# Kernel optimization log

Measured on AMD Instinct MI355X. Metric: run time of the kernel, lower is better.

The kernel has to match this reference:

```python
import jax, jax.numpy as jnp
import numpy as np

NUM_ITERATIONS = 3
EPS = 1e-12


def _squash(s):
    # s: (..., V). squash(s) = |s|^2 * s / ((1+|s|^2) * |s|)
    sq = jnp.sum(s * s, axis=-1, keepdims=True)
    return sq * s / ((1.0 + sq) * jnp.sqrt(sq))


def setup_inputs() -> dict:
    key = jax.random.key(0)
    kx, kw = jax.random.split(key)
    B, L, P, V, Q = 16, 64, 1024, 64, 16
    x = jax.random.normal(kx, (B, P, Q), dtype=jnp.float32)
    W = 0.01 * jax.random.normal(kw, (L, P, V, Q), dtype=jnp.float32)
    return {"x": x, "W": W}


def reference(x, W):
    # u_hat[b,l,p,v] = sum_q W[l,p,v,q] * x[b,p,q]
    u_hat = jnp.einsum('lpvq,bpq->blpv', W, x)  # (B, L, P, V)
    B, L, P, V = u_hat.shape
    b_ij = jnp.zeros((B, L, P), dtype=u_hat.dtype)
    c_ij = None
    v = None
    for it in range(NUM_ITERATIONS):  # small fixed unroll
        c_ij = jax.nn.softmax(b_ij, axis=1)  # softmax over latent caps
        s = jnp.einsum('blp,blpv->blv', c_ij, u_hat)
        v = _squash(s)  # (B, L, V)
        if it < NUM_ITERATIONS - 1:
            # agreement update: b_ij += <v_j, u_hat>
            b_ij = b_ij + jnp.einsum('blv,blpv->blp', v, u_hat)
    # T-score: coupling entropy over latent axis, per primary capsule
    cT = jnp.swapaxes(c_ij, 1, 2)  # (B, P, L)
    entropy = -jnp.sum(cT * jnp.log(cT + EPS), axis=-1)  # (B, P)
    T = jnp.mean(1.0 - entropy / np.log(float(L)))
    # D-score: max over caps of population std (over batch) of activation norms
    v_norm = jnp.linalg.norm(v, axis=-1)  # (B, L)
    D = jnp.max(jnp.std(v_norm, axis=0))
    return v, T, D
```

## Files before the change

kernel.cpp:

```cpp
#include <hip/hip_runtime.h>
#include <hip/hip_bf16.h>

#define B 16
#define L 64
#define P 1024
#define V 64
#define Q 16
#define LN64 4.158883083359672f

#define CHBC 16
#define NCH_BC (P / CHBC)

typedef unsigned short ushort8_t __attribute__((ext_vector_type(8)));

typedef const __attribute__((address_space(1))) void* gld_gptr_t;
typedef __attribute__((address_space(3))) void* gld_lptr_t;

static __device__ __forceinline__ float bf2f(ushort u) {
    return __uint_as_float(((unsigned int)u) << 16);
}
static __device__ __forceinline__ ushort f2bf(float f) {
    unsigned int x = __float_as_uint(f);
    unsigned int r = (x + 0x7fffu + ((x >> 16) & 1u)) >> 16;
    return (ushort)r;
}
static __device__ __forceinline__ float pklo(unsigned int w) {
    return __uint_as_float(w << 16);
}
static __device__ __forceinline__ float pkhi(unsigned int w) {
    return __uint_as_float(w & 0xffff0000u);
}

static __device__ __forceinline__ float wsum64(float v) {
#pragma unroll
    for (int m = 32; m > 0; m >>= 1) v += __shfl_xor(v, m, 64);
    return v;
}
static __device__ __forceinline__ float wmax64(float v) {
#pragma unroll
    for (int m = 32; m > 0; m >>= 1) v = fmaxf(v, __shfl_xor(v, m, 64));
    return v;
}

__global__ __launch_bounds__(256) void k_uhat(const float* __restrict__ Wt,
                                              const float* __restrict__ x,
                                              ushort* __restrict__ uhat) {
    const int t = threadIdx.x;
    const int w = t >> 6;
    const int lane = t & 63;
    const int p = blockIdx.x >> 1;
    const int l0 = (blockIdx.x & 1) * 32;

    __shared__ float xs[B * Q];
    __shared__ float wls[4][1024];

    {
        const int b = t >> 4, q = t & 15;
        xs[t] = x[((size_t)b * P + p) * Q + q];
    }
    __syncthreads();

    unsigned int xp[4][8];
#pragma unroll
    for (int i = 0; i < 4; ++i) {
        const int b = w * 4 + i;
#pragma unroll
        for (int j = 0; j < 8; ++j) {
            unsigned int lo = f2bf(xs[b * Q + 2 * j]);
            unsigned int hi = f2bf(xs[b * Q + 2 * j + 1]);
            xp[i][j] = lo | (hi << 16);
        }
    }

    const int i_idx = w * 64 + lane;
    const int src_chunk = (i_idx & ~3) | ((i_idx & 3) ^ ((i_idx >> 3) & 3));
    const char* gW = (const char*)Wt + ((size_t)l0 * P + p) * (V * Q * 4)
                     + (size_t)src_chunk * 16;
    const size_t LSTRIDE = (size_t)P * V * Q * 4;
    const int xsw = (lane >> 1) & 3;

#define STAGE(li)                                                             \
    __builtin_amdgcn_global_load_lds(                                         \
        (gld_gptr_t)(gW + (size_t)(li) * LSTRIDE),                            \
        (gld_lptr_t)&wls[(li) & 3][w * 256], 16, 0, 0);

#define COMPUTE(li)                                                           \
    {                                                                         \
        const char* sb = (const char*)&wls[(li) & 3][0] + lane * 64;          \
        float4 Wr[4];                                                         \
        Wr[0] = *(const float4*)(sb + ((0 ^ xsw) << 4));                      \
        Wr[1] = *(const float4*)(sb + ((1 ^ xsw) << 4));                      \
        Wr[2] = *(const float4*)(sb + ((2 ^ xsw) << 4));                      \
        Wr[3] = *(const float4*)(sb + ((3 ^ xsw) << 4));                      \
        _Pragma("unroll")                                                     \
        for (int i = 0; i < 4; ++i) {                                         \
            float u = 0.f;                                                    \
            _Pragma("unroll")                                                 \
            for (int j = 0; j < 8; ++j) {                                     \
                const float4 Wq = Wr[j >> 1];                                 \
                const float wlo = (j & 1) ? Wq.z : Wq.x;                      \
                const float whi = (j & 1) ? Wq.w : Wq.y;                      \
                u = fmaf(wlo, pklo(xp[i][j]), u);                             \
                u = fmaf(whi, pkhi(xp[i][j]), u);                             \
            }                                                                 \
            uhat[(((size_t)((w * 4 + i) * L + l0 + (li))) * P + p) * V + lane] \
                = f2bf(u);                                                    \
        }                                                                     \
    }

#define SYNC(N)                                                               \
    asm volatile("s_waitcnt vmcnt(" #N ")" ::: "memory");                     \
    __builtin_amdgcn_sched_barrier(0);                                        \
    __builtin_amdgcn_s_barrier();                                             \
    __builtin_amdgcn_sched_barrier(0);

    STAGE(0);
    STAGE(1);

    SYNC(1);
    STAGE(2);
    COMPUTE(0);
    SYNC(5);
    STAGE(3);
    COMPUTE(1);

#pragma unroll 1
    for (int li = 2; li <= 29; ++li) {
        SYNC(9);
        STAGE(li + 2);
        COMPUTE(li);
    }

    SYNC(9);
    COMPUTE(30);
    SYNC(8);
    COMPUTE(31);

#undef STAGE
#undef COMPUTE
#undef SYNC
}

__global__ __launch_bounds__(256) void k_s(const ushort* __restrict__ uhat,
                                           float* __restrict__ vout) {
    const int l = blockIdx.x, b = blockIdx.y;
    const int t = threadIdx.x;
    const int w = t >> 6, lane = t & 63;
    const int pl = t >> 4;
    const int vg = t & 15;

    __shared__ float4 sl[4][16];

    const ushort* up = uhat + ((size_t)(b * L + l)) * P * V + (size_t)pl * V + vg * 4;

    float4 acc = {0.f, 0.f, 0.f, 0.f};
#pragma unroll 8
    for (int i = 0; i < 64; ++i) {
        ushort4 u = *reinterpret_cast<const ushort4*>(up + (size_t)i * 16 * V);
        acc.x += bf2f(u.x); acc.y += bf2f(u.y);
        acc.z += bf2f(u.z); acc.w += bf2f(u.w);
    }
    acc.x *= (1.f / 64.f); acc.y *= (1.f / 64.f);
    acc.z *= (1.f / 64.f); acc.w *= (1.f / 64.f);
#pragma unroll
    for (int m = 16; m <= 32; m <<= 1) {
        acc.x += __shfl_xor(acc.x, m, 64);
        acc.y += __shfl_xor(acc.y, m, 64);
        acc.z += __shfl_xor(acc.z, m, 64);
        acc.w += __shfl_xor(acc.w, m, 64);
    }
    if (lane < 16) sl[w][vg] = acc;
    __syncthreads();
    if (w == 0 && lane < 16) {
        float4 s0 = sl[0][vg], s1 = sl[1][vg], s2 = sl[2][vg], s3 = sl[3][vg];
        float4 s;
        s.x = s0.x + s1.x + s2.x + s3.x;
        s.y = s0.y + s1.y + s2.y + s3.y;
        s.z = s0.z + s1.z + s2.z + s3.z;
        s.w = s0.w + s1.w + s2.w + s3.w;
        float sq = s.x * s.x + s.y * s.y + s.z * s.z + s.w * s.w;
        sq += __shfl_xor(sq, 1, 64);
        sq += __shfl_xor(sq, 2, 64);
        sq += __shfl_xor(sq, 4, 64);
        sq += __shfl_xor(sq, 8, 64);
        float f = sqrtf(sq) / (1.0f + sq);
        float4 o = {s.x * f, s.y * f, s.z * f, s.w * f};
        *reinterpret_cast<float4*>(vout + (size_t)(b * L + l) * V + vg * 4) = o;
    }
}

__global__ __launch_bounds__(512, 4) void k_bc(const ushort* __restrict__ uhat,
                                               const float* __restrict__ vv,
                                               float* __restrict__ bbuf,
                                               float* __restrict__ sp,
                                               float* __restrict__ Tsum,
                                               int add_prev, int do_T) {
    const int ch = blockIdx.x, b = blockIdx.y;
    const int p0 = ch * CHBC;
    const int t = threadIdx.x;
    const int w = t >> 6, lane = t & 63;
    const int pl8 = lane >> 3;
    const int vg8 = lane & 7;
    const int l0 = w * 8;

    __shared__ float vsh[L][V];
    __shared__ float bl[CHBC][L + 1];
    __shared__ float twv[8];

    {
        const float4* vvp = reinterpret_cast<const float4*>(vv + (size_t)b * L * V);
        float4* vshp = reinterpret_cast<float4*>(&vsh[0][0]);
#pragma unroll
        for (int i = 0; i < 2; ++i) vshp[t + i * 512] = vvp[t + i * 512];
    }

    ushort8_t ur[8][2];
    {
        const ushort* ubase = uhat + (((size_t)(b * L + l0)) * P + p0 + pl8) * V + vg8 * 8;
#pragma unroll
        for (int li = 0; li < 8; ++li) {
#pragma unroll
            for (int ph = 0; ph < 2; ++ph)
                ur[li][ph] = *reinterpret_cast<const ushort8_t*>(
                    ubase + ((size_t)li * P + ph * 8) * V);
        }
    }
    __syncthreads();

#pragma unroll
    for (int li = 0; li < 8; ++li) {
        const int l = l0 + li;
        const float4 va = *reinterpret_cast<const float4*>(&vsh[l][vg8 * 8]);
        const float4 vb = *reinterpret_cast<const float4*>(&vsh[l][vg8 * 8 + 4]);
#pragma unroll
        for (int ph = 0; ph < 2; ++ph) {
            float d;
            d = bf2f(ur[li][ph][0]) * va.x;
            d = fmaf(bf2f(ur[li][ph][1]), va.y, d);
            d = fmaf(bf2f(ur[li][ph][2]), va.z, d);
            d = fmaf(bf2f(ur[li][ph][3]), va.w, d);
            d = fmaf(bf2f(ur[li][ph][4]), vb.x, d);
            d = fmaf(bf2f(ur[li][ph][5]), vb.y, d);
            d = fmaf(bf2f(ur[li][ph][6]), vb.z, d);
            d = fmaf(bf2f(ur[li][ph][7]), vb.w, d);
            d += __shfl_xor(d, 1, 64);
            d += __shfl_xor(d, 2, 64);
            d += __shfl_xor(d, 4, 64);
            if (vg8 == 0) bl[ph * 8 + pl8][l] = d;
        }
    }
    __syncthreads();

    float tloc = 0.f;
#pragma unroll
    for (int pi = 0; pi < 2; ++pi) {
        const int pli = w * 2 + pi;
        const int p = p0 + pli;
        float bv = bl[pli][lane];
        float* bp = bbuf + ((size_t)b * P + p) * L;
        if (add_prev) bv += bp[lane];
        bp[lane] = bv;
        float m = wmax64(bv);
        float e = __expf(bv - m);
        float ssum = wsum64(e);
        float cc = e / ssum;
        bl[pli][lane] = cc;
        if (do_T) tloc += cc * __logf(64.0f * (cc + 1e-12f));
    }
    if (do_T) {
        float dsum = wsum64(tloc);
        if (lane == 0) twv[w] = dsum;
    }
    __syncthreads();
    if (do_T && t == 0) {
        float s8 = twv[0] + twv[1] + twv[2] + twv[3] +
                   twv[4] + twv[5] + twv[6] + twv[7];
        atomicAdd(Tsum, s8 * (1.0f / LN64));
    }

    float* spb = sp + (size_t)(b * NCH_BC + ch) * L * V;
#pragma unroll
    for (int li = 0; li < 8; ++li) {
        const int l = l0 + li;
        const float cA = bl[pl8][l];
        const float cB = bl[8 + pl8][l];
        float4 pa, pb;
        pa.x = cA * bf2f(ur[li][0][0]) + cB * bf2f(ur[li][1][0]);
        pa.y = cA * bf2f(ur[li][0][1]) + cB * bf2f(ur[li][1][1]);
        pa.z = cA * bf2f(ur[li][0][2]) + cB * bf2f(ur[li][1][2]);
        pa.w = cA * bf2f(ur[li][0][3]) + cB * bf2f(ur[li][1][3]);
        pb.x = cA * bf2f(ur[li][0][4]) + cB * bf2f(ur[li][1][4]);
        pb.y = cA * bf2f(ur[li][0][5]) + cB * bf2f(ur[li][1][5]);
        pb.z = cA * bf2f(ur[li][0][6]) + cB * bf2f(ur[li][1][6]);
        pb.w = cA * bf2f(ur[li][0][7]) + cB * bf2f(ur[li][1][7]);
#pragma unroll
        for (int m = 8; m <= 32; m <<= 1) {
            pa.x += __shfl_xor(pa.x, m, 64);
            pa.y += __shfl_xor(pa.y, m, 64);
            pa.z += __shfl_xor(pa.z, m, 64);
            pa.w += __shfl_xor(pa.w, m, 64);
            pb.x += __shfl_xor(pb.x, m, 64);
            pb.y += __shfl_xor(pb.y, m, 64);
            pb.z += __shfl_xor(pb.z, m, 64);
            pb.w += __shfl_xor(pb.w, m, 64);
        }
        if (pl8 == 0) {
            *reinterpret_cast<float4*>(spb + (size_t)l * V + vg8 * 8) = pa;
            *reinterpret_cast<float4*>(spb + (size_t)l * V + vg8 * 8 + 4) = pb;
        }
    }
}

__global__ __launch_bounds__(256) void k_v(const float* __restrict__ sp,
                                           float* __restrict__ vout,
                                           float* __restrict__ norms) {
    const int b = blockIdx.y;
    const int w = threadIdx.x >> 6, lane = threadIdx.x & 63;
    const int l = blockIdx.x * 4 + w;
    const float* p = sp + ((size_t)b * NCH_BC * L + l) * V + lane;
    float s = 0.f;
#pragma unroll 8
    for (int ch = 0; ch < NCH_BC; ++ch) s += p[(size_t)ch * L * V];
    float sq = wsum64(s * s);
    float f = sqrtf(sq) / (1.0f + sq);
    vout[((size_t)b * L + l) * V + lane] = s * f;
    if (norms && lane == 0) norms[b * L + l] = sq / (1.0f + sq);
}

__global__ void k_final(const float* __restrict__ Tsum,
                        const float* __restrict__ norms,
                        float* __restrict__ out) {
    const int lane = threadIdx.x & 63;
    float n[B];
    float sum = 0.f;
#pragma unroll
    for (int b = 0; b < B; ++b) { n[b] = norms[b * L + lane]; sum += n[b]; }
    const float mean = sum * (1.0f / B);
    float var = 0.f;
#pragma unroll
    for (int b = 0; b < B; ++b) { float d = n[b] - mean; var = fmaf(d, d, var); }
    var *= (1.0f / B);
    float sd = sqrtf(var);
    float D = wmax64(sd);
    if (lane == 0) {
        out[B * L * V] = Tsum[0] * (1.0f / (B * P));
        out[B * L * V + 1] = D;
    }
}

extern "C" void kernel_launch(void* const* d_in, const int* in_sizes, int n_in,
                              void* d_out, int out_size, void* d_ws, size_t ws_size,
                              hipStream_t stream) {
    const float* x = (const float*)d_in[0];
    const float* W = (const float*)d_in[1];
    float* out = (float*)d_out;

    char* ws = (char*)d_ws;
    ushort* uhat = (ushort*)ws;
    size_t off = (size_t)B * L * P * V * 2;
    float* spbuf = (float*)(ws + off); off += (size_t)B * NCH_BC * L * V * 4;
    float* vbuf  = (float*)(ws + off); off += (size_t)B * L * V * 4;
    float* bbuf  = (float*)(ws + off); off += (size_t)B * P * L * 4;
    float* norms = (float*)(ws + off); off += (size_t)B * L * 4;
    float* Tsum  = (float*)(ws + off); off += 256;

    hipMemsetAsync(Tsum, 0, sizeof(float), stream);

    hipLaunchKernelGGL(k_uhat, dim3(2048), dim3(256), 0, stream, W, x, uhat);
    hipLaunchKernelGGL(k_s, dim3(L, B), dim3(256), 0, stream, uhat, vbuf);
    hipLaunchKernelGGL(k_bc, dim3(NCH_BC, B), dim3(512), 0, stream,
                       uhat, vbuf, bbuf, spbuf, Tsum, 0, 0);
    hipLaunchKernelGGL(k_v, dim3(L / 4, B), dim3(256), 0, stream,
                       spbuf, vbuf, (float*)nullptr);
    hipLaunchKernelGGL(k_bc, dim3(NCH_BC, B), dim3(512), 0, stream,
                       uhat, vbuf, bbuf, spbuf, Tsum, 1, 1);
    hipLaunchKernelGGL(k_v, dim3(L / 4, B), dim3(256), 0, stream,
                       spbuf, out, norms);
    hipLaunchKernelGGL(k_final, dim3(1), dim3(64), 0, stream, Tsum, norms, out);
}
```

Baseline: 228.5 us.

## Make k_uhat waves independent with private 6-deep LDS ring and deferred stores

Each wave now loads only its own 16-wide slice of V for every latent cap into a private 6-stage LDS ring, so the block-wide s_barrier is dropped and only per-wave vmcnt waits remain. The wave-to-work mapping changes from 4 batches × 64 v per wave to 16 batches (4 per lane group) × 16 v per wave. All 32 u_hat results are held in registers and written at the end instead of being interleaved with the loads. The cost is much higher register use (32 uint2 per thread) and more LDS (24 KB), which can lower occupancy, and the final 2-byte stores are scattered rather than coalesced.

```diff
diff --git a/kernel.cpp b/kernel.cpp
--- a/kernel.cpp
+++ b/kernel.cpp
@@ -48,11 +48,13 @@
     const int t = threadIdx.x;
     const int w = t >> 6;
     const int lane = t & 63;
+    const int bq = lane >> 4;
+    const int vl = lane & 15;
     const int p = blockIdx.x >> 1;
     const int l0 = (blockIdx.x & 1) * 32;
 
     __shared__ float xs[B * Q];
-    __shared__ float wls[4][1024];
+    __shared__ char wls[4][6][1024];
 
     {
         const int b = t >> 4, q = t & 15;
@@ -63,7 +65,7 @@
     unsigned int xp[4][8];
 #pragma unroll
     for (int i = 0; i < 4; ++i) {
-        const int b = w * 4 + i;
+        const int b = bq * 4 + i;
 #pragma unroll
         for (int j = 0; j < 8; ++j) {
             unsigned int lo = f2bf(xs[b * Q + 2 * j]);
@@ -72,26 +74,29 @@
         }
     }
 
-    const int i_idx = w * 64 + lane;
-    const int src_chunk = (i_idx & ~3) | ((i_idx & 3) ^ ((i_idx >> 3) & 3));
+    const int c = (lane & ~3) | ((lane & 3) ^ ((lane >> 3) & 3));
     const char* gW = (const char*)Wt + ((size_t)l0 * P + p) * (V * Q * 4)
-                     + (size_t)src_chunk * 16;
+                     + w * 1024 + c * 16;
     const size_t LSTRIDE = (size_t)P * V * Q * 4;
-    const int xsw = (lane >> 1) & 3;
+    char* wbase = &wls[w][0][0];
+    const int xsw = (vl >> 1) & 3;
+
+    uint2 uout[32];
 
 #define STAGE(li)                                                             \
     __builtin_amdgcn_global_load_lds(                                         \
         (gld_gptr_t)(gW + (size_t)(li) * LSTRIDE),                            \
-        (gld_lptr_t)&wls[(li) & 3][w * 256], 16, 0, 0);
+        (gld_lptr_t)(wbase + ((li) % 6) * 1024), 16, 0, 0);
 
 #define COMPUTE(li)                                                           \
     {                                                                         \
-        const char* sb = (const char*)&wls[(li) & 3][0] + lane * 64;          \
+        const char* sb = wbase + ((li) % 6) * 1024 + vl * 64;                 \
         float4 Wr[4];                                                         \
         Wr[0] = *(const float4*)(sb + ((0 ^ xsw) << 4));                      \
         Wr[1] = *(const float4*)(sb + ((1 ^ xsw) << 4));                      \
         Wr[2] = *(const float4*)(sb + ((2 ^ xsw) << 4));                      \
         Wr[3] = *(const float4*)(sb + ((3 ^ xsw) << 4));                      \
+        float uu[4];                                                          \
         _Pragma("unroll")                                                     \
         for (int i = 0; i < 4; ++i) {                                         \
             float u = 0.f;                                                    \
@@ -103,42 +108,49 @@
                 u = fmaf(wlo, pklo(xp[i][j]), u);                             \
                 u = fmaf(whi, pkhi(xp[i][j]), u);                             \
             }                                                                 \
-            uhat[(((size_t)((w * 4 + i) * L + l0 + (li))) * P + p) * V + lane] \
-                = f2bf(u);                                                    \
+            uu[i] = u;                                                        \
         }                                                                     \
-    }
-
-#define SYNC(N)                                                               \
+        uout[li].x = (unsigned)f2bf(uu[0]) | ((unsigned)f2bf(uu[1]) << 16);   \
+        uout[li].y = (unsigned)f2bf(uu[2]) | ((unsigned)f2bf(uu[3]) << 16);   \
+    }
+
+#define WAITV(N)                                                              \
     asm volatile("s_waitcnt vmcnt(" #N ")" ::: "memory");                     \
-    __builtin_amdgcn_sched_barrier(0);                                        \
-    __builtin_amdgcn_s_barrier();                                             \
     __builtin_amdgcn_sched_barrier(0);
 
     STAGE(0);
     STAGE(1);
-
-    SYNC(1);
     STAGE(2);
-    COMPUTE(0);
-    SYNC(5);
     STAGE(3);
-    COMPUTE(1);
-
-#pragma unroll 1
-    for (int li = 2; li <= 29; ++li) {
-        SYNC(9);
-        STAGE(li + 2);
+    STAGE(4);
+
+#pragma unroll
+    for (int li = 0; li < 27; ++li) {
+        WAITV(4);
+        STAGE(li + 5);
         COMPUTE(li);
     }
-
-    SYNC(9);
-    COMPUTE(30);
-    SYNC(8);
-    COMPUTE(31);
+    WAITV(4); COMPUTE(27);
+    WAITV(3); COMPUTE(28);
+    WAITV(2); COMPUTE(29);
+    WAITV(1); COMPUTE(30);
+    WAITV(0); COMPUTE(31);
+
+    const int v = w * 16 + vl;
+#pragma unroll
+    for (int li = 0; li < 32; ++li) {
+#pragma unroll
+        for (int i = 0; i < 4; ++i) {
+            const int b = bq * 4 + i;
+            const unsigned pairv = (i >> 1) ? uout[li].y : uout[li].x;
+            const ushort us = (ushort)((i & 1) ? (pairv >> 16) : (pairv & 0xffffu));
+            uhat[(((size_t)(b * L + l0 + li)) * P + p) * V + v] = us;
+        }
+    }
 
 #undef STAGE
 #undef COMPUTE
-#undef SYNC
+#undef WAITV
 }
 
 __global__ __launch_bounds__(256) void k_s(const ushort* __restrict__ uhat,
```

Result: slower. 290.6 us (+27.2%).
